# Performance work log

Hardware: AMD Instinct MI355X
Metric: run time of the kernel (lower is better)

## Reference

```python
import jax, jax.numpy as jnp
import numpy as np

B, L_IN, D = 4, 4096, 1024
R_MIN, R_MAX = 0.9, 0.999


def setup_inputs() -> dict:
    key = jax.random.key(0)
    k0, k1, k2 = jax.random.split(key, 3)
    inputs = jax.random.normal(k0, (B, L_IN, D), jnp.float32)
    Wi = jax.random.normal(k1, (2 * D, D), jnp.float32) / np.sqrt(D)
    bi = jnp.zeros((2 * D,), jnp.float32)
    Wo = jax.random.normal(k2, (D, 2 * D), jnp.float32) / np.sqrt(2 * D)
    bo = jnp.zeros((D,), jnp.float32)
    # LRU stable-ring initialization, exactly as in the torch module
    rng = np.random.default_rng(0)
    u1 = rng.random(D)
    u2 = rng.random(D)
    v_log = np.log(-0.5 * np.log(u1 * (R_MAX ** 2 - R_MIN ** 2) + R_MIN ** 2))
    theta_log = np.log(u2 * np.pi * 2)
    gamma_log = np.log(np.sqrt(1.0 - np.exp(-np.exp(v_log)) ** 2))
    params_log = jnp.asarray(np.stack([v_log, theta_log, gamma_log]), jnp.float32)
    return {"inputs": inputs, "Wi": Wi, "bi": bi, "Wo": Wo, "bo": bo,
            "params_log": params_log}


def _lru_forward(inputs, Wi, bi, Wo, bo, params_log):
    b, l_in, d = inputs.shape
    u = inputs @ Wi.T + bi                      # [B, L, 2D]
    v, theta, gamma = jnp.exp(params_log)       # each [D]
    # torch.view_as_complex: interleaved (real, imag) pairs along last dim
    uc = u.reshape(b, l_in, d, 2)
    x = jax.lax.complex(uc[..., 0], uc[..., 1])  # [B, L, D] complex64
    log2_L = int(np.ceil(np.log2(l_in)))
    L = 2 ** log2_L
    x = jnp.pad(x, ((0, 0), (0, L - l_in), (0, 0)))
    # Blelloch-style log-depth scan: x_t = lambda * x_{t-1} + u_t,
    # lambda = exp(-v + i*theta)
    for i in range(1, log2_L + 1):
        blk = 2 ** i
        xb = x.reshape(b * L // blk, blk, d)
        x1, x2 = xb[:, : blk // 2], xb[:, blk // 2:]
        pos = jnp.arange(1, blk // 2 + 1, dtype=jnp.float32)  # [blk/2]
        lambs = jnp.exp(jax.lax.complex(-pos[:, None] * v,
                                        pos[:, None] * theta))  # [blk/2, D]
        x2 = x2 + lambs * x1[:, -1:]
        x = jnp.concatenate([x1, x2], axis=1).reshape(b, L, d)
    x = x[:, :l_in] * gamma.astype(x.dtype)     # normalize, drop padding
    xr = jnp.concatenate([x.real, x.imag], axis=-1)  # [B, L, 2D]
    out = xr @ Wo.T + bo
    return jax.nn.relu(out)


def reference(inputs, Wi, bi, Wo, bo, params_log):
    return _lru_forward(inputs, Wi, bi, Wo, bo, params_log)
```

## Files before the change

kernel.cpp:

```cpp
#include <hip/hip_runtime.h>
#include <hip/hip_cooperative_groups.h>

#define BB 4
#define LL 4096
#define DD 1024
#define SS 64
#define TT 64

typedef __attribute__((ext_vector_type(4))) float  floatx4;
typedef __attribute__((ext_vector_type(8))) short  shortx8;
typedef __attribute__((ext_vector_type(8))) unsigned short ushortx8;

static __device__ __forceinline__ unsigned short f2bf(float f) {
    unsigned int u = __float_as_uint(f);
    u += 0x7fffu + ((u >> 16) & 1u);
    return (unsigned short)(u >> 16);
}
static __device__ __forceinline__ float bf2f(unsigned short h) {
    return __uint_as_float(((unsigned int)h) << 16);
}

#define NIN4 (BB * LL * DD / 4)
#define NWI4 (2 * DD * DD / 4)
#define NWO8 (DD * DD / 4)
__global__ void cast_all_kernel(const float4* __restrict__ s_in, ushort4* __restrict__ d_inb,
                                const float4* __restrict__ s_wi, ushort4* __restrict__ d_wib,
                                const float* __restrict__ s_wo, unsigned short* __restrict__ d_wob) {
    int i = blockIdx.x * blockDim.x + threadIdx.x;
    if (i < NIN4 + NWI4) {
        const float4* s; ushort4* d; int j;
        if (i < NIN4) { s = s_in; d = d_inb; j = i; }
        else          { s = s_wi; d = d_wib; j = i - NIN4; }
        float4 v = s[j];
        ushort4 o;
        o.x = f2bf(v.x); o.y = f2bf(v.y); o.z = f2bf(v.z); o.w = f2bf(v.w);
        d[j] = o;
    } else {
        int j = i - NIN4 - NWI4;
        int n  = j >> 8;
        int d0 = (j & 255) * 4;
        const float* rowp = s_wo + (size_t)n * (2 * DD);
        float4 re = *(const float4*)(rowp + d0);
        float4 im = *(const float4*)(rowp + DD + d0);
        ushortx8 o;
        o[0] = f2bf(re.x); o[1] = f2bf(im.x);
        o[2] = f2bf(re.y); o[3] = f2bf(im.y);
        o[4] = f2bf(re.z); o[5] = f2bf(im.z);
        o[6] = f2bf(re.w); o[7] = f2bf(im.w);
        *(ushortx8*)(d_wob + (size_t)n * (2 * DD) + 2 * d0) = o;
    }
}

template<int K, int NT, int EPI>
__global__ __launch_bounds__(512, 2)
void gemm256(const unsigned short* __restrict__ A,
             const unsigned short* __restrict__ B,
             const float* __restrict__ bias,
             void* __restrict__ Cp) {
    constexpr int N   = NT * 256;
    constexpr int NKT = K / 64;
    __shared__ __align__(16) short As[2][256 * 64];
    __shared__ __align__(16) short Bs[2][256 * 64];

    const int tid = threadIdx.x;
    const int blk = blockIdx.x;
    const int xcd = blk & 7;
    const int i2  = blk >> 3;
    const int tileM = ((i2 / NT) * 8 + xcd) * 256;
    const int tileN = (i2 % NT) * 256;

    const int lane   = tid & 63;
    const int wave   = tid >> 6;
    const int wave_m = wave >> 2;
    const int wave_n = wave & 3;
    const int r16    = lane & 15;
    const int quad   = lane >> 4;
    const int slotx  = r16 & 7;
    const int wmRow  = wave_m * 64 + r16;
    const int wnRow  = wave_n * 32 + r16;

    const int srow = tid >> 3;
    const int scol = ((tid & 7) ^ (srow & 7)) * 8;
    const int ldsChunkBase = (tid & ~63) * 8;
    const size_t aOff = (size_t)(tileM + srow) * K + scol;
    const size_t bOff = (size_t)(tileN + srow) * K + scol;

    floatx4 acc[8][4] = {};
    shortx8 af[4][2], bf0v[2][2], bf1v[2][2];

#define GLL(SRC, DST) __builtin_amdgcn_global_load_lds( \
        (const __attribute__((address_space(1))) void*)(SRC), \
        (__attribute__((address_space(3))) void*)(DST), 16, 0, 0)
#define STAGE_A(BUF, H, KT) do { \
    GLL(A + aOff + (size_t)((H) * 128) * K + (KT) * 64,      &As[BUF][(H) * 8192 + ldsChunkBase]); \
    GLL(A + aOff + (size_t)((H) * 128 + 64) * K + (KT) * 64, &As[BUF][(H) * 8192 + 4096 + ldsChunkBase]); \
} while (0)
#define STAGE_B(BUF, H, KT) do { \
    GLL(B + bOff + (size_t)((H) * 128) * K + (KT) * 64,      &Bs[BUF][(H) * 8192 + ldsChunkBase]); \
    GLL(B + bOff + (size_t)((H) * 128 + 64) * K + (KT) * 64, &Bs[BUF][(H) * 8192 + 4096 + ldsChunkBase]); \
} while (0)
#define LOAD_A(BUF, MH) do { \
    _Pragma("unroll") for (int il = 0; il < 4; ++il) \
    _Pragma("unroll") for (int kk = 0; kk < 2; ++kk) \
        af[il][kk] = *(const shortx8*)&As[BUF][((MH) * 128 + wmRow + il * 16) * 64 + ((kk * 4 + quad) ^ slotx) * 8]; \
} while (0)
#define LOAD_B(BUF, NH, DST) do { \
    _Pragma("unroll") for (int jl = 0; jl < 2; ++jl) \
    _Pragma("unroll") for (int kk = 0; kk < 2; ++kk) \
        DST[jl][kk] = *(const shortx8*)&Bs[BUF][((NH) * 128 + wnRow + jl * 16) * 64 + ((kk * 4 + quad) ^ slotx) * 8]; \
} while (0)
#define MFMAQ(MH, NH, BF) do { \
    __builtin_amdgcn_s_setprio(1); \
    _Pragma("unroll") for (int kk = 0; kk < 2; ++kk) \
    _Pragma("unroll") for (int il = 0; il < 4; ++il) \
    _Pragma("unroll") for (int jl = 0; jl < 2; ++jl) \
        acc[(MH) * 4 + il][(NH) * 2 + jl] = __builtin_amdgcn_mfma_f32_16x16x32_bf16( \
            af[il][kk], BF[jl][kk], acc[(MH) * 4 + il][(NH) * 2 + jl], 0, 0, 0); \
    __builtin_amdgcn_s_setprio(0); \
} while (0)
#define BAR()  __builtin_amdgcn_s_barrier()
#define LGKM0() asm volatile("s_waitcnt lgkmcnt(0)" ::: "memory")

    STAGE_A(0, 0, 0);
    STAGE_B(0, 0, 0);
    STAGE_B(0, 1, 0);
    STAGE_A(0, 1, 0);
    STAGE_A(1, 0, 1);
    STAGE_B(1, 1, 1);
    STAGE_A(1, 1, 1);
    asm volatile("s_waitcnt vmcnt(6)" ::: "memory");
    BAR();
    LOAD_A(0, 0);
    LOAD_B(0, 0, bf0v);

#pragma unroll 2
    for (int t = 0; t < NKT; ++t) {
        const int cb = t & 1;
        const int t1 = (t + 1 < NKT) ? t + 1 : NKT - 1;
        const int t2 = (t + 2 < NKT) ? t + 2 : NKT - 1;
        BAR();
        LGKM0();
        STAGE_B(cb ^ 1, 0, t1);
        MFMAQ(0, 0, bf0v);
        LOAD_B(cb, 1, bf1v);
        BAR();
        LGKM0();
        STAGE_A(cb, 0, t2);
        MFMAQ(0, 1, bf1v);
        LOAD_A(cb, 1);
        BAR();
        LGKM0();
        STAGE_B(cb, 1, t2);
        MFMAQ(1, 0, bf0v);
        asm volatile("s_waitcnt vmcnt(4)" ::: "memory");
        BAR();
        STAGE_A(cb, 1, t2);
        MFMAQ(1, 1, bf1v);
        LOAD_A(cb ^ 1, 0);
        LOAD_B(cb ^ 1, 0, bf0v);
    }
    asm volatile("s_waitcnt vmcnt(0) lgkmcnt(0)" ::: "memory");

#pragma unroll
    for (int i = 0; i < 8; ++i) {
        const int row0 = tileM + (i >> 2) * 128 + wave_m * 64 + (i & 3) * 16 + quad * 4;
#pragma unroll
        for (int j = 0; j < 4; ++j) {
            const int col = tileN + (j >> 1) * 128 + wave_n * 32 + (j & 1) * 16 + r16;
            const float bv = bias[col];
#pragma unroll
            for (int r = 0; r < 4; ++r) {
                float v = acc[i][j][r] + bv;
                if (EPI == 0) {
                    ((unsigned short*)Cp)[(size_t)(row0 + r) * N + col] = f2bf(v);
                } else {
                    ((float*)Cp)[(size_t)(row0 + r) * N + col] = fmaxf(v, 0.0f);
                }
            }
        }
    }
#undef GLL
#undef STAGE_A
#undef STAGE_B
#undef LOAD_A
#undef LOAD_B
#undef MFMAQ
#undef BAR
#undef LGKM0
}

__global__ __launch_bounds__(256, 4)
void scan_fused(const unsigned short* __restrict__ u,
                const float* __restrict__ plog,
                float2* __restrict__ E,
                unsigned short* __restrict__ xr) {
    const int d = blockIdx.x * 256 + threadIdx.x;
    const int c = blockIdx.y, b = blockIdx.z;

    unsigned int w[TT];
    {
        const unsigned short* up = u + (size_t)(b * LL + c * TT) * (2 * DD) + 2 * d;
#pragma unroll
        for (int tl = 0; tl < TT; ++tl) { w[tl] = *(const unsigned int*)up; up += 2 * DD; }
    }
    {
        const float v  = expf(plog[d]);
        const float th = expf(plog[DD + d]);
        const float a  = expf(-v);
        const float lr = a * cosf(th), li = a * sinf(th);
        float zr = 0.f, zi = 0.f;
#pragma unroll
        for (int tl = 0; tl < TT; ++tl) {
            float xv = bf2f((unsigned short)(w[tl] & 0xffffu));
            float yv = bf2f((unsigned short)(w[tl] >> 16));
            float t = lr * zr - li * zi + xv;
            zi = lr * zi + li * zr + yv;
            zr = t;
        }
        E[(size_t)c * (BB * DD) + b * DD + d] = make_float2(zr, zi);
    }
    __threadfence();
    cooperative_groups::this_grid().sync();

    if (c == 0) {
        const float v  = expf(plog[d]);
        const float th = expf(plog[DD + d]);
        const float aT = expf(-(float)TT * v);
        const float Lr = aT * cosf((float)TT * th), Li = aT * sinf((float)TT * th);
        float yr = 0.f, yi = 0.f;
        float2* p = E + (size_t)b * DD + d;
#pragma unroll 8
        for (int cc = 0; cc < SS; ++cc) {
            float2 e = *p;
            *p = make_float2(yr, yi);
            float t = Lr * yr - Li * yi + e.x;
            yi = Lr * yi + Li * yr + e.y;
            yr = t;
            p += BB * DD;
        }
    }
    __threadfence();
    cooperative_groups::this_grid().sync();

    {
        const float v  = expf(plog[d]);
        const float th = expf(plog[DD + d]);
        const float g  = expf(plog[2 * DD + d]);
        const float a  = expf(-v);
        const float lr = a * cosf(th), li = a * sinf(th);
        const float2 cy = E[(size_t)c * (BB * DD) + b * DD + d];
        float yr = cy.x, yi = cy.y;
        unsigned short* xp = xr + (size_t)(b * LL + c * TT) * (2 * DD) + 2 * d;
#pragma unroll
        for (int tl = 0; tl < TT; ++tl) {
            float xv = bf2f((unsigned short)(w[tl] & 0xffffu));
            float yv = bf2f((unsigned short)(w[tl] >> 16));
            float t = lr * yr - li * yi + xv;
            yi = lr * yi + li * yr + yv;
            yr = t;
            *(unsigned int*)xp = (unsigned int)f2bf(g * yr) |
                                 ((unsigned int)f2bf(g * yi) << 16);
            xp += 2 * DD;
        }
    }
}

__global__ __launch_bounds__(256)
void scanA(const unsigned short* __restrict__ u,
           const float* __restrict__ plog,
           float2* __restrict__ Eend) {
    const int d = blockIdx.x * 256 + threadIdx.x;
    const int c = blockIdx.y, b = blockIdx.z;
    const float v  = expf(plog[d]);
    const float th = expf(plog[DD + d]);
    const float a  = expf(-v);
    const float lr = a * cosf(th), li = a * sinf(th);
    float zr = 0.f, zi = 0.f;
    const unsigned short* up = u + (size_t)(b * LL + c * TT) * (2 * DD) + 2 * d;
#pragma unroll 8
    for (int tl = 0; tl < TT; ++tl) {
        unsigned int pr = *(const unsigned int*)up;
        float xr = bf2f((unsigned short)(pr & 0xffffu));
        float xi = bf2f((unsigned short)(pr >> 16));
        float t = lr * zr - li * zi + xr;
        zi = lr * zi + li * zr + xi;
        zr = t;
        up += 2 * DD;
    }
    Eend[(size_t)c * (BB * DD) + b * DD + d] = make_float2(zr, zi);
}

__global__ __launch_bounds__(256)
void scanB(const float* __restrict__ plog, float2* __restrict__ E) {
    const int i = blockIdx.x * 256 + threadIdx.x;
    const int d = i & (DD - 1);
    const float v  = expf(plog[d]);
    const float th = expf(plog[DD + d]);
    const float aT = expf(-(float)TT * v);
    const float Lr = aT * cosf((float)TT * th), Li = aT * sinf((float)TT * th);
    float yr = 0.f, yi = 0.f;
    float2* p = E + i;
#pragma unroll 8
    for (int c = 0; c < SS; ++c) {
        float2 e = *p;
        *p = make_float2(yr, yi);
        float t = Lr * yr - Li * yi + e.x;
        yi = Lr * yi + Li * yr + e.y;
        yr = t;
        p += BB * DD;
    }
}

__global__ __launch_bounds__(256)
void scanC(const unsigned short* __restrict__ u,
           const float* __restrict__ plog,
           const float2* __restrict__ Carry,
           unsigned short* __restrict__ xr) {
    const int d = blockIdx.x * 256 + threadIdx.x;
    const int c = blockIdx.y, b = blockIdx.z;
    const float v  = expf(plog[d]);
    const float th = expf(plog[DD + d]);
    const float g  = expf(plog[2 * DD + d]);
    const float a  = expf(-v);
    const float lr = a * cosf(th), li = a * sinf(th);
    const float2 cy = Carry[(size_t)c * (BB * DD) + b * DD + d];
    float yr = cy.x, yi = cy.y;
    const unsigned short* up = u + (size_t)(b * LL + c * TT) * (2 * DD) + 2 * d;
    unsigned short* xp = xr + (size_t)(b * LL + c * TT) * (2 * DD) + 2 * d;
#pragma unroll 8
    for (int tl = 0; tl < TT; ++tl) {
        unsigned int pr = *(const unsigned int*)up;
        float xrv = bf2f((unsigned short)(pr & 0xffffu));
        float xiv = bf2f((unsigned short)(pr >> 16));
        float t = lr * yr - li * yi + xrv;
        yi = lr * yi + li * yr + xiv;
        yr = t;
        *(unsigned int*)xp = (unsigned int)f2bf(g * yr) |
                             ((unsigned int)f2bf(g * yi) << 16);
        up += 2 * DD;
        xp += 2 * DD;
    }
}

extern "C" void kernel_launch(void* const* d_in, const int* in_sizes, int n_in,
                              void* d_out, int out_size, void* d_ws, size_t ws_size,
                              hipStream_t stream) {
    const float* inputs = (const float*)d_in[0];
    const float* Wi     = (const float*)d_in[1];
    const float* bi     = (const float*)d_in[2];
    const float* Wo     = (const float*)d_in[3];
    const float* bo     = (const float*)d_in[4];
    const float* plog   = (const float*)d_in[5];
    float* out = (float*)d_out;

    const size_t M = (size_t)BB * LL;
    unsigned short* u_bf  = (unsigned short*)d_ws;
    unsigned short* xr_bf = u_bf  + M * 2 * DD;
    unsigned short* in_bf = xr_bf + M * 2 * DD;
    unsigned short* Wi_bf = in_bf + M * DD;
    unsigned short* Wo_bf = Wi_bf + (size_t)2 * DD * DD;
    float2* Eend = (float2*)in_bf;

    {
        int total = NIN4 + NWI4 + NWO8;
        cast_all_kernel<<<total / 256, 256, 0, stream>>>(
            (const float4*)inputs, (ushort4*)in_bf,
            (const float4*)Wi,     (ushort4*)Wi_bf,
            Wo,                    Wo_bf);
    }

    gemm256<DD, 8, 0><<<(M / 256) * 8, 512, 0, stream>>>(
        in_bf, Wi_bf, bi, (void*)u_bf);

    bool coop = false;
    {
        int nb = 0;
        hipError_t qe = hipOccupancyMaxActiveBlocksPerMultiprocessor(&nb, scan_fused, 256, 0);
        if (qe == hipSuccess && nb >= 4) {
            const unsigned short* u_arg = u_bf;
            const float* p_arg = plog;
            float2* e_arg = Eend;
            unsigned short* x_arg = xr_bf;
            void* args[] = { (void*)&u_arg, (void*)&p_arg, (void*)&e_arg, (void*)&x_arg };
            hipError_t le = hipLaunchCooperativeKernel(scan_fused,
                dim3(DD / 256, SS, BB), dim3(256), args, 0, stream);
            coop = (le == hipSuccess);
        }
    }
    if (!coop) {
        scanA<<<dim3(DD / 256, SS, BB), 256, 0, stream>>>(u_bf, plog, Eend);
        scanB<<<(BB * DD) / 256, 256, 0, stream>>>(plog, Eend);
        scanC<<<dim3(DD / 256, SS, BB), 256, 0, stream>>>(u_bf, plog, Eend, xr_bf);
    }

    gemm256<2 * DD, 4, 1><<<(M / 256) * 4, 512, 0, stream>>>(
        xr_bf, Wo_bf, bo, (void*)out);
}
```

Before: 293.9 us.

## Replace cooperative grid syncs with flag-based decoupled chunk-carry scan

Swaps the cooperative-launch scan, which used two grid-wide barriers and a serial carry pass by chunk 0, for a one-pass kernel. Each block publishes its chunk-end state with an atomic store and sets a per-chunk flag, then waits on the flags of earlier chunks in its chain and combines their states itself. This removes the grid-wide synchronisations and the cooperative launch overhead, at the cost of O(c) redundant combine work per block and spin-waiting. It depends on all blocks being co-resident to avoid deadlock; the occupancy check is meant to guarantee this. Flags are reset inside the cast kernel.

```diff
diff --git a/kernel.cpp b/kernel.cpp
--- a/kernel.cpp
+++ b/kernel.cpp
@@ -1,11 +1,11 @@
 #include <hip/hip_runtime.h>
-#include <hip/hip_cooperative_groups.h>
 
 #define BB 4
 #define LL 4096
 #define DD 1024
 #define SS 64
 #define TT 64
+#define NCH 16
 
 typedef __attribute__((ext_vector_type(4))) float  floatx4;
 typedef __attribute__((ext_vector_type(8))) short  shortx8;
@@ -25,8 +25,10 @@
 #define NWO8 (DD * DD / 4)
 __global__ void cast_all_kernel(const float4* __restrict__ s_in, ushort4* __restrict__ d_inb,
                                 const float4* __restrict__ s_wi, ushort4* __restrict__ d_wib,
-                                const float* __restrict__ s_wo, unsigned short* __restrict__ d_wob) {
+                                const float* __restrict__ s_wo, unsigned short* __restrict__ d_wob,
+                                int* __restrict__ flags) {
     int i = blockIdx.x * blockDim.x + threadIdx.x;
+    if (i < NCH * SS) flags[i] = 0;
     if (i < NIN4 + NWI4) {
         const float4* s; ushort4* d; int j;
         if (i < NIN4) { s = s_in; d = d_inb; j = i; }
@@ -190,12 +192,14 @@
 }
 
 __global__ __launch_bounds__(256, 4)
-void scan_fused(const unsigned short* __restrict__ u,
-                const float* __restrict__ plog,
-                float2* __restrict__ E,
-                unsigned short* __restrict__ xr) {
+void scan_onepass(const unsigned short* __restrict__ u,
+                  const float* __restrict__ plog,
+                  unsigned long long* __restrict__ Epub,
+                  int* __restrict__ flags,
+                  unsigned short* __restrict__ xr) {
     const int d = blockIdx.x * 256 + threadIdx.x;
     const int c = blockIdx.y, b = blockIdx.z;
+    const int chain = b * (DD / 256) + blockIdx.x;
 
     unsigned int w[TT];
     {
@@ -203,11 +207,15 @@
 #pragma unroll
         for (int tl = 0; tl < TT; ++tl) { w[tl] = *(const unsigned int*)up; up += 2 * DD; }
     }
+    const float v  = expf(plog[d]);
+    const float th = expf(plog[DD + d]);
+    const float g  = expf(plog[2 * DD + d]);
+    const float a  = expf(-v);
+    const float lr = a * cosf(th), li = a * sinf(th);
+    const float aT = expf(-(float)TT * v);
+    const float Lr = aT * cosf((float)TT * th), Li = aT * sinf((float)TT * th);
+
     {
-        const float v  = expf(plog[d]);
-        const float th = expf(plog[DD + d]);
-        const float a  = expf(-v);
-        const float lr = a * cosf(th), li = a * sinf(th);
         float zr = 0.f, zi = 0.f;
 #pragma unroll
         for (int tl = 0; tl < TT; ++tl) {
@@ -217,39 +225,59 @@
             zi = lr * zi + li * zr + yv;
             zr = t;
         }
-        E[(size_t)c * (BB * DD) + b * DD + d] = make_float2(zr, zi);
+        unsigned long long q = (unsigned long long)__float_as_uint(zr) |
+                               ((unsigned long long)__float_as_uint(zi) << 32);
+        __hip_atomic_store(&Epub[(size_t)c * (BB * DD) + b * DD + d], q,
+                           __ATOMIC_RELAXED, __HIP_MEMORY_SCOPE_AGENT);
     }
     __threadfence();
-    cooperative_groups::this_grid().sync();
-
-    if (c == 0) {
-        const float v  = expf(plog[d]);
-        const float th = expf(plog[DD + d]);
-        const float aT = expf(-(float)TT * v);
-        const float Lr = aT * cosf((float)TT * th), Li = aT * sinf((float)TT * th);
-        float yr = 0.f, yi = 0.f;
-        float2* p = E + (size_t)b * DD + d;
-#pragma unroll 8
-        for (int cc = 0; cc < SS; ++cc) {
-            float2 e = *p;
-            *p = make_float2(yr, yi);
-            float t = Lr * yr - Li * yi + e.x;
-            yi = Lr * yi + Li * yr + e.y;
-            yr = t;
-            p += BB * DD;
+    __syncthreads();
+    if (threadIdx.x == 0)
+        __hip_atomic_store(&flags[chain * SS + c], 1,
+                           __ATOMIC_RELEASE, __HIP_MEMORY_SCOPE_AGENT);
+
+    float yr = 0.f, yi = 0.f;
+    if (c > 0) {
+        const int fbase = chain * SS;
+        if ((threadIdx.x & 63) == 0) {
+            for (int j0 = 0; j0 < c; j0 += 8) {
+                for (;;) {
+                    int got = 0;
+#pragma unroll
+                    for (int k = 0; k < 8; ++k) {
+                        got += (j0 + k >= c) ? 1 :
+                            (__hip_atomic_load(&flags[fbase + j0 + k],
+                                 __ATOMIC_ACQUIRE, __HIP_MEMORY_SCOPE_AGENT) != 0);
+                    }
+                    if (got == 8) break;
+                    __builtin_amdgcn_s_sleep(2);
+                }
+            }
         }
-    }
-    __threadfence();
-    cooperative_groups::this_grid().sync();
+        const size_t pbase = (size_t)b * DD + d;
+        int j = 0;
+#define PLD(JJ) __hip_atomic_load(&Epub[(size_t)(JJ) * (BB * DD) + pbase], \
+                                  __ATOMIC_RELAXED, __HIP_MEMORY_SCOPE_AGENT)
+#define COMB(Q) do { \
+        float er = __uint_as_float((unsigned int)(Q)); \
+        float ei = __uint_as_float((unsigned int)((Q) >> 32)); \
+        float t = Lr * yr - Li * yi + er; \
+        yi = Lr * yi + Li * yr + ei; \
+        yr = t; } while (0)
+        for (; j + 8 <= c; j += 8) {
+            unsigned long long q0 = PLD(j + 0), q1 = PLD(j + 1);
+            unsigned long long q2 = PLD(j + 2), q3 = PLD(j + 3);
+            unsigned long long q4 = PLD(j + 4), q5 = PLD(j + 5);
+            unsigned long long q6 = PLD(j + 6), q7 = PLD(j + 7);
+            COMB(q0); COMB(q1); COMB(q2); COMB(q3);
+            COMB(q4); COMB(q5); COMB(q6); COMB(q7);
+        }
+        for (; j < c; ++j) { unsigned long long q = PLD(j); COMB(q); }
+#undef PLD
+#undef COMB
+    }
 
     {
-        const float v  = expf(plog[d]);
-        const float th = expf(plog[DD + d]);
-        const float g  = expf(plog[2 * DD + d]);
-        const float a  = expf(-v);
-        const float lr = a * cosf(th), li = a * sinf(th);
-        const float2 cy = E[(size_t)c * (BB * DD) + b * DD + d];
-        float yr = cy.x, yi = cy.y;
         unsigned short* xp = xr + (size_t)(b * LL + c * TT) * (2 * DD) + 2 * d;
 #pragma unroll
         for (int tl = 0; tl < TT; ++tl) {
@@ -359,35 +387,36 @@
     unsigned short* in_bf = xr_bf + M * 2 * DD;
     unsigned short* Wi_bf = in_bf + M * DD;
     unsigned short* Wo_bf = Wi_bf + (size_t)2 * DD * DD;
+    unsigned long long* Epub = (unsigned long long*)in_bf;
     float2* Eend = (float2*)in_bf;
+    int* flags = (int*)(Wo_bf + (size_t)2 * DD * DD);
 
     {
         int total = NIN4 + NWI4 + NWO8;
         cast_all_kernel<<<total / 256, 256, 0, stream>>>(
             (const float4*)inputs, (ushort4*)in_bf,
             (const float4*)Wi,     (ushort4*)Wi_bf,
-            Wo,                    Wo_bf);
+            Wo,                    Wo_bf,
+            flags);
     }
 
     gemm256<DD, 8, 0><<<(M / 256) * 8, 512, 0, stream>>>(
         in_bf, Wi_bf, bi, (void*)u_bf);
 
-    bool coop = false;
-    {
+    static int onepass_ok = -1;
+    if (onepass_ok < 0) {
         int nb = 0;
-        hipError_t qe = hipOccupancyMaxActiveBlocksPerMultiprocessor(&nb, scan_fused, 256, 0);
-        if (qe == hipSuccess && nb >= 4) {
-            const unsigned short* u_arg = u_bf;
-            const float* p_arg = plog;
-            float2* e_arg = Eend;
-            unsigned short* x_arg = xr_bf;
-            void* args[] = { (void*)&u_arg, (void*)&p_arg, (void*)&e_arg, (void*)&x_arg };
-            hipError_t le = hipLaunchCooperativeKernel(scan_fused,
-                dim3(DD / 256, SS, BB), dim3(256), args, 0, stream);
-            coop = (le == hipSuccess);
-        }
-    }
-    if (!coop) {
+        hipError_t qe = hipOccupancyMaxActiveBlocksPerMultiprocessor(
+            &nb, (const void*)scan_onepass, 256, 0);
+        hipFuncAttributes attr{};
+        hipError_t ae = hipFuncGetAttributes(&attr, (const void*)scan_onepass);
+        onepass_ok = (qe == hipSuccess && nb >= 4 &&
+                      ae == hipSuccess && attr.localSizeBytes == 0) ? 1 : 0;
+    }
+    if (onepass_ok) {
+        scan_onepass<<<dim3(DD / 256, SS, BB), 256, 0, stream>>>(
+            u_bf, plog, Epub, flags, xr_bf);
+    } else {
         scanA<<<dim3(DD / 256, SS, BB), 256, 0, stream>>>(u_bf, plog, Eend);
         scanB<<<(BB * DD) / 256, 256, 0, stream>>>(plog, Eend);
         scanC<<<dim3(DD / 256, SS, BB), 256, 0, stream>>>(u_bf, plog, Eend, xr_bf);
```

New measurement: 290.9 us. About the same (-1.0%).
